# Kernel tuning notes

Measured on AMD Instinct MI355X. Metric: run time of the kernel, lower is better.

## Reference

```python
import math
import jax, jax.numpy as jnp
import numpy as np

B, T, J, EMBED, W = 16, 243, 17, 256, 3  # D = EMBED + 1 = 257, KW = 2*W+1 = 7


def log_map0_spatial(x):
    """Lorentz log map at origin (curvature 1), returning the spatial part.
    x: [..., d+1] points on the hyperboloid. Equals log_map0(x)[..., 1:]."""
    x_t = x[..., :1]
    x_s = x[..., 1:]
    xn = jnp.clip(jnp.linalg.norm(x_s, axis=-1, keepdims=True), 1e-7, None)
    return jnp.arccosh(jnp.maximum(x_t, 1.0 + 1e-7)) / xn * x_s


def exp_map0(v):
    """Lorentz exp map at origin. v: [..., d+1] tangent vector (time comp 0)."""
    v_s = v[..., 1:]
    n = jnp.clip(jnp.linalg.norm(v_s, axis=-1, keepdims=True), 1e-7, None)
    return jnp.concatenate([jnp.cosh(n), jnp.sinh(n) / n * v_s], axis=-1)


def setup_inputs() -> dict:
    key = jax.random.key(0)
    ks = jax.random.split(key, 8)
    # valid hyperboloid points: time = sqrt(1 + ||spatial||^2)
    s = jax.random.normal(ks[0], (B, T, J, EMBED), jnp.float32) * 0.5
    t = jnp.sqrt(1.0 + jnp.sum(s * s, axis=-1, keepdims=True))
    x_seq = jnp.concatenate([t, s], axis=-1)  # [B,T,J,D]
    vel_seq = jax.random.normal(ks[1], (B, T, J, EMBED + 1), jnp.float32) * 0.1
    sc = 1.0 / math.sqrt(EMBED)
    Wq = jax.random.normal(ks[2], (EMBED, EMBED), jnp.float32) * sc
    Wk = jax.random.normal(ks[3], (EMBED, EMBED), jnp.float32) * sc
    Wv = jax.random.normal(ks[4], (EMBED, EMBED), jnp.float32) * sc
    bq = jax.random.normal(ks[5], (EMBED,), jnp.float32) * sc
    bk = jax.random.normal(ks[6], (EMBED,), jnp.float32) * sc
    bv = jax.random.normal(ks[7], (EMBED,), jnp.float32) * sc
    tau = jnp.ones((1,), jnp.float32)
    return {"x_seq": x_seq, "vel_seq": vel_seq, "tau": tau,
            "Wq": Wq, "bq": bq, "Wk": Wk, "bk": bk, "Wv": Wv, "bv": bv}


def reference(x_seq, vel_seq, tau, Wq, bq, Wk, bk, Wv, bv):
    Bb, Tt, Jj, D = x_seq.shape
    d = D - 1
    KW = 2 * W + 1
    # [B,T,J,D] -> [B*J, T, D]
    x_flat = jnp.transpose(x_seq, (0, 2, 1, 3)).reshape(Bb * Jj, Tt, D)
    spatial = log_map0_spatial(x_flat)  # [BJ, T, d]
    q = spatial @ Wq.T + bq
    k = spatial @ Wk.T + bk
    v = spatial @ Wv.T + bv
    # replicate-pad along time, build +/-W windows (fixed small loop over KW=7)
    k_pad = jnp.pad(k, ((0, 0), (W, W), (0, 0)), mode='edge')
    v_pad = jnp.pad(v, ((0, 0), (W, W), (0, 0)), mode='edge')
    k_win = jnp.stack([k_pad[:, i:i + Tt] for i in range(KW)], axis=2)  # [BJ,T,KW,d]
    v_win = jnp.stack([v_pad[:, i:i + Tt] for i in range(KW)], axis=2)
    tau_c = jnp.maximum(tau, 0.001)  # shape [1], broadcasts
    logits = jnp.einsum('btd,btwd->btw', q, k_win) / (math.sqrt(d) * tau_c)
    # mask out-of-range frames at the temporal boundaries
    frame_idx = jnp.arange(Tt)[:, None] + (jnp.arange(KW) - W)[None, :]
    boundary = (frame_idx < 0) | (frame_idx >= Tt)  # [T,KW]
    logits = jnp.where(boundary[None], -jnp.inf, logits)
    attn = jax.nn.softmax(logits, axis=-1)  # [BJ,T,KW]
    agg = jnp.einsum('btw,btwd->btd', attn, v_win)  # [BJ,T,d]
    agg_full = jnp.pad(agg, ((0, 0), (0, 0), (1, 0)))  # prepend zero time comp
    z = exp_map0(agg_full)  # [BJ,T,D]
    return jnp.transpose(z.reshape(Bb, Jj, Tt, D), (0, 2, 1, 3))
```

## Files before the change

### kernel.cpp

```cpp
#include <hip/hip_runtime.h>
#include <hip/hip_bf16.h>

#define B_   16
#define T_   243
#define J_   17
#define E_   256
#define D_   257
#define BJ_  (B_ * J_)
#define M_   (BJ_ * T_)

typedef __bf16 bf16x8 __attribute__((ext_vector_type(8)));
typedef float  f32x4  __attribute__((ext_vector_type(4)));

static __device__ __forceinline__ float bf2f(unsigned short u) {
  unsigned int v = ((unsigned int)u) << 16;
  return __builtin_bit_cast(float, v);
}
static __device__ __forceinline__ unsigned short f2bf(float f) {
  __hip_bfloat16 h = __float2bfloat16(f);
  return __builtin_bit_cast(unsigned short, h);
}
static __device__ __forceinline__ float wave_sum(float v) {
  v += __shfl_xor(v, 1);
  v += __shfl_xor(v, 2);
  v += __shfl_xor(v, 4);
  v += __shfl_xor(v, 8);
  v += __shfl_xor(v, 16);
  v += __shfl_xor(v, 32);
  return v;
}
static __device__ __forceinline__ void gload_lds16(const void* g, void* l) {
  __builtin_amdgcn_global_load_lds(
      (const __attribute__((address_space(1))) void*)g,
      (__attribute__((address_space(3))) void*)l, 16, 0, 0);
}

__global__ void fuse_w_kernel(const float* __restrict__ Wq,
                              const float* __restrict__ Wk,
                              const float* __restrict__ Wv,
                              __hip_bfloat16* __restrict__ wf) {
  int idx = blockIdx.x * 256 + threadIdx.x;
  float v = (idx < 65536) ? Wq[idx]
          : (idx < 131072) ? Wk[idx - 65536]
                           : Wv[idx - 131072];
  ((unsigned short*)wf)[idx] = f2bf(v);
}

__global__ __launch_bounds__(512) void qkv_fused_kernel(
    const float* __restrict__ x, const unsigned short* __restrict__ Wf,
    const float* __restrict__ bq, const float* __restrict__ bk,
    const float* __restrict__ bv, unsigned short* __restrict__ C) {
  __shared__ __align__(16) unsigned short lA[128 * 256];
  __shared__ __align__(16) unsigned short lW[2][128 * 64];

  int tid  = threadIdx.x;
  int w    = tid >> 6;
  int lane = tid & 63;
  int wr   = w >> 2;
  int wcn  = w & 3;
  int m0   = blockIdx.x * 128;

  {
    char* bA = (char*)lA;
    for (int rr = 0; rr < 16; ++rr) {
      int lr = w * 16 + rr;
      int m  = m0 + lr; if (m > M_ - 1) m = M_ - 1;
      int bj = m / T_;  int t = m - bj * T_;
      int b  = bj / J_; int j = bj - b * J_;
      const float* row = x + (size_t)((b * T_ + t) * J_ + j) * D_;
      float xs[4], ss = 0.f;
#pragma unroll
      for (int i = 0; i < 4; ++i) {
        xs[i] = row[1 + lane * 4 + i];
        ss += xs[i] * xs[i];
      }
      ss = wave_sum(ss);
      float xn = fmaxf(sqrtf(ss), 1e-7f);
      float alpha = acoshf(fmaxf(row[0], 1.f + 1e-7f)) / xn;
      ushort4 o;
      o.x = f2bf(xs[0] * alpha); o.y = f2bf(xs[1] * alpha);
      o.z = f2bf(xs[2] * alpha); o.w = f2bf(xs[3] * alpha);
      int byte = lr * 512 + ((lane * 8) ^ ((lr & 7) << 4));
      *(ushort4*)(bA + byte) = o;
    }
  }
  __syncthreads();

  int rowInWave = lane >> 3;
  int srcSlot   = (lane & 7) ^ rowInWave;

  const char* bA = (const char*)lA;

  for (int nt = 0; nt < 6; ++nt) {
    int n0 = nt * 128;

    float bias[2];
#pragma unroll
    for (int ni = 0; ni < 2; ++ni) {
      int colg = n0 + wcn * 32 + ni * 16 + (lane & 15);
      bias[ni] = (colg < 256) ? bq[colg]
               : (colg < 512) ? bk[colg - 256] : bv[colg - 512];
    }

    f32x4 acc[4][2] = {};

#pragma unroll
    for (int i = 0; i < 2; ++i) {
      int rbase = (w * 2 + i) * 8;
      gload_lds16(Wf + (size_t)(n0 + rbase + rowInWave) * 256 + srcSlot * 8,
                  lW[0] + rbase * 64);
    }
    __syncthreads();

    for (int kk = 0; kk < 4; ++kk) {
      if (kk < 3) {
#pragma unroll
        for (int i = 0; i < 2; ++i) {
          int rbase = (w * 2 + i) * 8;
          gload_lds16(Wf + (size_t)(n0 + rbase + rowInWave) * 256 +
                          (kk + 1) * 64 + srcSlot * 8,
                      lW[(kk + 1) & 1] + rbase * 64);
        }
      }
      const char* bW = (const char*)lW[kk & 1];
#pragma unroll
      for (int ki = 0; ki < 2; ++ki) {
        bf16x8 a[4], bfr[2];
        int cbA = kk * 128 + ki * 64 + (lane >> 4) * 16;
#pragma unroll
        for (int mi = 0; mi < 4; ++mi) {
          int r = wr * 64 + mi * 16 + (lane & 15);
          a[mi] = *(const bf16x8*)(bA + r * 512 + (cbA ^ ((r & 7) << 4)));
        }
        int cbB = ki * 64 + (lane >> 4) * 16;
#pragma unroll
        for (int ni = 0; ni < 2; ++ni) {
          int r = wcn * 32 + ni * 16 + (lane & 15);
          bfr[ni] = *(const bf16x8*)(bW + r * 128 + (cbB ^ ((r & 7) << 4)));
        }
#pragma unroll
        for (int mi = 0; mi < 4; ++mi)
#pragma unroll
          for (int ni = 0; ni < 2; ++ni)
            acc[mi][ni] = __builtin_amdgcn_mfma_f32_16x16x32_bf16(
                a[mi], bfr[ni], acc[mi][ni], 0, 0, 0);
      }
      __syncthreads();
    }

    char* bC = (char*)lW[0];
#pragma unroll
    for (int mi = 0; mi < 4; ++mi)
#pragma unroll
      for (int ni = 0; ni < 2; ++ni) {
        int col = wcn * 32 + ni * 16 + (lane & 15);
#pragma unroll
        for (int r = 0; r < 4; ++r) {
          int row  = wr * 64 + mi * 16 + (lane >> 4) * 4 + r;
          int byte = row * 256 + ((col * 2) ^ ((row & 7) << 4));
          *(unsigned short*)(bC + byte) = f2bf(acc[mi][ni][r] + bias[ni]);
        }
      }
    __syncthreads();
#pragma unroll
    for (int p = 0; p < 4; ++p) {
      int row  = p * 32 + (tid >> 4);
      int seg  = tid & 15;
      int byte = row * 256 + ((seg * 16) ^ ((row & 7) << 4));
      uint4 val = *(const uint4*)(bC + byte);
      int gm = m0 + row;
      if (gm < M_)
        *(uint4*)(C + (size_t)gm * 768 + n0 + seg * 8) = val;
    }
    __syncthreads();
  }
}

__global__ __launch_bounds__(256) void attn_kernel(
    const unsigned short* __restrict__ qkv, const float* __restrict__ tau,
    float* __restrict__ out) {
  int wid  = threadIdx.x >> 6;
  int lane = threadIdx.x & 63;
  int t = blockIdx.x * 4 + wid;
  if (t >= T_) return;
  int bj = blockIdx.y;
  int b = bj / J_, j = bj % J_;
  size_t mrow = (size_t)bj * T_ + t;

  float tauc = fmaxf(tau[0], 1e-3f);
  float sc = 1.f / (16.f * tauc);

  float q[4];
  {
    ushort4 qa = *(const ushort4*)(qkv + mrow * 768 + lane * 4);
    q[0] = bf2f(qa.x); q[1] = bf2f(qa.y); q[2] = bf2f(qa.z); q[3] = bf2f(qa.w);
  }

  float logit[7];
#pragma unroll
  for (int ww = 0; ww < 7; ++ww) {
    int t2 = t + ww - 3;
    float d = -INFINITY;
    if (t2 >= 0 && t2 < T_) {
      size_t m2 = (size_t)bj * T_ + t2;
      ushort4 ka = *(const ushort4*)(qkv + m2 * 768 + 256 + lane * 4);
      float p = q[0] * bf2f(ka.x) + q[1] * bf2f(ka.y) +
                q[2] * bf2f(ka.z) + q[3] * bf2f(ka.w);
      d = wave_sum(p) * sc;
    }
    logit[ww] = d;
  }

  float mx = logit[0];
#pragma unroll
  for (int ww = 1; ww < 7; ++ww) mx = fmaxf(mx, logit[ww]);
  float e[7], s = 0.f;
#pragma unroll
  for (int ww = 0; ww < 7; ++ww) {
    e[ww] = expf(logit[ww] - mx);
    s += e[ww];
  }
  float inv = 1.f / s;

  float agg[4] = {0.f, 0.f, 0.f, 0.f};
#pragma unroll
  for (int ww = 0; ww < 7; ++ww) {
    int t2 = t + ww - 3;
    if (t2 >= 0 && t2 < T_) {
      size_t m2 = (size_t)bj * T_ + t2;
      ushort4 va = *(const ushort4*)(qkv + m2 * 768 + 512 + lane * 4);
      agg[0] += e[ww] * bf2f(va.x);
      agg[1] += e[ww] * bf2f(va.y);
      agg[2] += e[ww] * bf2f(va.z);
      agg[3] += e[ww] * bf2f(va.w);
    }
  }
#pragma unroll
  for (int i = 0; i < 4; ++i) agg[i] *= inv;

  float nn = agg[0]*agg[0] + agg[1]*agg[1] + agg[2]*agg[2] + agg[3]*agg[3];
  nn = wave_sum(nn);
  float n = fmaxf(sqrtf(nn), 1e-7f);
  float scale = sinhf(n) / n;

  float* orow = out + ((size_t)(b * T_ + t) * J_ + j) * D_;
  if (lane == 0) orow[0] = coshf(n);
#pragma unroll
  for (int i = 0; i < 4; ++i) orow[1 + lane * 4 + i] = agg[i] * scale;
}

extern "C" void kernel_launch(void* const* d_in, const int* in_sizes, int n_in,
                              void* d_out, int out_size, void* d_ws, size_t ws_size,
                              hipStream_t stream) {
  const float* x   = (const float*)d_in[0];
  const float* tau = (const float*)d_in[2];
  const float* Wq  = (const float*)d_in[3];
  const float* bq  = (const float*)d_in[4];
  const float* Wk  = (const float*)d_in[5];
  const float* bk  = (const float*)d_in[6];
  const float* Wv  = (const float*)d_in[7];
  const float* bv  = (const float*)d_in[8];
  float* out = (float*)d_out;

  char* ws = (char*)d_ws;
  __hip_bfloat16* wf  = (__hip_bfloat16*)(ws);
  unsigned short* qkv = (unsigned short*)(ws + 393216);

  fuse_w_kernel<<<dim3(768), dim3(256), 0, stream>>>(Wq, Wk, Wv, wf);
  qkv_fused_kernel<<<dim3(517), dim3(512), 0, stream>>>(
      x, (const unsigned short*)wf, bq, bk, bv, qkv);
  attn_kernel<<<dim3(61, BJ_), dim3(256), 0, stream>>>(qkv, tau, out);
}
```

Baseline: 343.3 us.

## Halve GEMM row tile and loop attention waves over 16 timesteps

The QKV GEMM now uses 64-row tiles with 256 threads, doubling the grid so more CUs get work and each block needs less LDS. The attention kernel gives each wave a run of 16 consecutive timesteps, clamps window indices so it can load all K and V rows without branches, and writes the output as float4. Reloading overlapping window rows within one wave is meant to hit cache and cut launch overhead, but the attention grid shrinks to 4x272 blocks with a serial loop, which may underfill the GPU.

```diff
diff --git a/kernel.cpp b/kernel.cpp
--- a/kernel.cpp
+++ b/kernel.cpp
@@ -46,19 +46,19 @@
   ((unsigned short*)wf)[idx] = f2bf(v);
 }
 
-__global__ __launch_bounds__(512) void qkv_fused_kernel(
+__global__ __launch_bounds__(256) void qkv_gemm_kernel(
     const float* __restrict__ x, const unsigned short* __restrict__ Wf,
     const float* __restrict__ bq, const float* __restrict__ bk,
     const float* __restrict__ bv, unsigned short* __restrict__ C) {
-  __shared__ __align__(16) unsigned short lA[128 * 256];
+  __shared__ __align__(16) unsigned short lA[64 * 256];
   __shared__ __align__(16) unsigned short lW[2][128 * 64];
 
   int tid  = threadIdx.x;
   int w    = tid >> 6;
   int lane = tid & 63;
-  int wr   = w >> 2;
-  int wcn  = w & 3;
-  int m0   = blockIdx.x * 128;
+  int wr   = w >> 1;
+  int wcn  = w & 1;
+  int m0   = blockIdx.x * 64;
 
   {
     char* bA = (char*)lA;
@@ -94,19 +94,19 @@
   for (int nt = 0; nt < 6; ++nt) {
     int n0 = nt * 128;
 
-    float bias[2];
-#pragma unroll
-    for (int ni = 0; ni < 2; ++ni) {
-      int colg = n0 + wcn * 32 + ni * 16 + (lane & 15);
+    float bias[4];
+#pragma unroll
+    for (int ni = 0; ni < 4; ++ni) {
+      int colg = n0 + wcn * 64 + ni * 16 + (lane & 15);
       bias[ni] = (colg < 256) ? bq[colg]
                : (colg < 512) ? bk[colg - 256] : bv[colg - 512];
     }
 
-    f32x4 acc[4][2] = {};
-
-#pragma unroll
-    for (int i = 0; i < 2; ++i) {
-      int rbase = (w * 2 + i) * 8;
+    f32x4 acc[2][4] = {};
+
+#pragma unroll
+    for (int i = 0; i < 4; ++i) {
+      int rbase = (w * 4 + i) * 8;
       gload_lds16(Wf + (size_t)(n0 + rbase + rowInWave) * 256 + srcSlot * 8,
                   lW[0] + rbase * 64);
     }
@@ -115,8 +115,8 @@
     for (int kk = 0; kk < 4; ++kk) {
       if (kk < 3) {
 #pragma unroll
-        for (int i = 0; i < 2; ++i) {
-          int rbase = (w * 2 + i) * 8;
+        for (int i = 0; i < 4; ++i) {
+          int rbase = (w * 4 + i) * 8;
           gload_lds16(Wf + (size_t)(n0 + rbase + rowInWave) * 256 +
                           (kk + 1) * 64 + srcSlot * 8,
                       lW[(kk + 1) & 1] + rbase * 64);
@@ -125,23 +125,23 @@
       const char* bW = (const char*)lW[kk & 1];
 #pragma unroll
       for (int ki = 0; ki < 2; ++ki) {
-        bf16x8 a[4], bfr[2];
+        bf16x8 a[2], bfr[4];
         int cbA = kk * 128 + ki * 64 + (lane >> 4) * 16;
 #pragma unroll
-        for (int mi = 0; mi < 4; ++mi) {
-          int r = wr * 64 + mi * 16 + (lane & 15);
+        for (int mi = 0; mi < 2; ++mi) {
+          int r = wr * 32 + mi * 16 + (lane & 15);
           a[mi] = *(const bf16x8*)(bA + r * 512 + (cbA ^ ((r & 7) << 4)));
         }
         int cbB = ki * 64 + (lane >> 4) * 16;
 #pragma unroll
-        for (int ni = 0; ni < 2; ++ni) {
-          int r = wcn * 32 + ni * 16 + (lane & 15);
+        for (int ni = 0; ni < 4; ++ni) {
+          int r = wcn * 64 + ni * 16 + (lane & 15);
           bfr[ni] = *(const bf16x8*)(bW + r * 128 + (cbB ^ ((r & 7) << 4)));
         }
 #pragma unroll
-        for (int mi = 0; mi < 4; ++mi)
-#pragma unroll
-          for (int ni = 0; ni < 2; ++ni)
+        for (int mi = 0; mi < 2; ++mi)
+#pragma unroll
+          for (int ni = 0; ni < 4; ++ni)
             acc[mi][ni] = __builtin_amdgcn_mfma_f32_16x16x32_bf16(
                 a[mi], bfr[ni], acc[mi][ni], 0, 0, 0);
       }
@@ -150,13 +150,13 @@
 
     char* bC = (char*)lW[0];
 #pragma unroll
-    for (int mi = 0; mi < 4; ++mi)
-#pragma unroll
-      for (int ni = 0; ni < 2; ++ni) {
-        int col = wcn * 32 + ni * 16 + (lane & 15);
+    for (int mi = 0; mi < 2; ++mi)
+#pragma unroll
+      for (int ni = 0; ni < 4; ++ni) {
+        int col = wcn * 64 + ni * 16 + (lane & 15);
 #pragma unroll
         for (int r = 0; r < 4; ++r) {
-          int row  = wr * 64 + mi * 16 + (lane >> 4) * 4 + r;
+          int row  = wr * 32 + mi * 16 + (lane >> 4) * 4 + r;
           int byte = row * 256 + ((col * 2) ^ ((row & 7) << 4));
           *(unsigned short*)(bC + byte) = f2bf(acc[mi][ni][r] + bias[ni]);
         }
@@ -164,7 +164,7 @@
     __syncthreads();
 #pragma unroll
     for (int p = 0; p < 4; ++p) {
-      int row  = p * 32 + (tid >> 4);
+      int row  = p * 16 + (tid >> 4);
       int seg  = tid & 15;
       int byte = row * 256 + ((seg * 16) ^ ((row & 7) << 4));
       uint4 val = *(const uint4*)(bC + byte);
@@ -181,72 +181,70 @@
     float* __restrict__ out) {
   int wid  = threadIdx.x >> 6;
   int lane = threadIdx.x & 63;
-  int t = blockIdx.x * 4 + wid;
-  if (t >= T_) return;
+  int c  = blockIdx.x * 4 + wid;
+  int t0 = c * 16;
+  int t1 = min(T_, t0 + 16);
   int bj = blockIdx.y;
   int b = bj / J_, j = bj % J_;
-  size_t mrow = (size_t)bj * T_ + t;
+  const unsigned short* base = qkv + (size_t)bj * T_ * 768;
 
   float tauc = fmaxf(tau[0], 1e-3f);
   float sc = 1.f / (16.f * tauc);
 
-  float q[4];
-  {
-    ushort4 qa = *(const ushort4*)(qkv + mrow * 768 + lane * 4);
-    q[0] = bf2f(qa.x); q[1] = bf2f(qa.y); q[2] = bf2f(qa.z); q[3] = bf2f(qa.w);
+  for (int t = t0; t < t1; ++t) {
+    ushort4 qa = *(const ushort4*)(base + (size_t)t * 768 + lane * 4);
+    ushort4 ka[7], va[7];
+#pragma unroll
+    for (int ww = 0; ww < 7; ++ww) {
+      int t2 = t + ww - 3;
+      int tc = min(max(t2, 0), T_ - 1);
+      const unsigned short* rowp = base + (size_t)tc * 768;
+      ka[ww] = *(const ushort4*)(rowp + 256 + lane * 4);
+      va[ww] = *(const ushort4*)(rowp + 512 + lane * 4);
+    }
+    float q0 = bf2f(qa.x), q1 = bf2f(qa.y), q2 = bf2f(qa.z), q3 = bf2f(qa.w);
+
+    float logit[7];
+#pragma unroll
+    for (int ww = 0; ww < 7; ++ww) {
+      float p = q0 * bf2f(ka[ww].x) + q1 * bf2f(ka[ww].y) +
+                q2 * bf2f(ka[ww].z) + q3 * bf2f(ka[ww].w);
+      p = wave_sum(p) * sc;
+      int t2 = t + ww - 3;
+      logit[ww] = (t2 < 0 || t2 >= T_) ? -INFINITY : p;
+    }
+
+    float mx = logit[0];
+#pragma unroll
+    for (int ww = 1; ww < 7; ++ww) mx = fmaxf(mx, logit[ww]);
+    float e[7], s = 0.f;
+#pragma unroll
+    for (int ww = 0; ww < 7; ++ww) {
+      e[ww] = expf(logit[ww] - mx);
+      s += e[ww];
+    }
+    float inv = 1.f / s;
+
+    float ag0 = 0.f, ag1 = 0.f, ag2 = 0.f, ag3 = 0.f;
+#pragma unroll
+    for (int ww = 0; ww < 7; ++ww) {
+      ag0 += e[ww] * bf2f(va[ww].x);
+      ag1 += e[ww] * bf2f(va[ww].y);
+      ag2 += e[ww] * bf2f(va[ww].z);
+      ag3 += e[ww] * bf2f(va[ww].w);
+    }
+    ag0 *= inv; ag1 *= inv; ag2 *= inv; ag3 *= inv;
+
+    float nn = wave_sum(ag0*ag0 + ag1*ag1 + ag2*ag2 + ag3*ag3);
+    float n = fmaxf(sqrtf(nn), 1e-7f);
+    float scale = sinhf(n) / n;
+
+    float* orow = out + ((size_t)(b * T_ + t) * J_ + j) * D_;
+    if (lane == 0) orow[0] = coshf(n);
+    float4 o; o.x = ag0 * scale; o.y = ag1 * scale;
+    o.z = ag2 * scale; o.w = ag3 * scale;
+    *(float4*)(orow + 1 + lane * 4) = o;
   }
-
-  float logit[7];
-#pragma unroll
-  for (int ww = 0; ww < 7; ++ww) {
-    int t2 = t + ww - 3;
-    float d = -INFINITY;
-    if (t2 >= 0 && t2 < T_) {
-      size_t m2 = (size_t)bj * T_ + t2;
-      ushort4 ka = *(const ushort4*)(qkv + m2 * 768 + 256 + lane * 4);
-      float p = q[0] * bf2f(ka.x) + q[1] * bf2f(ka.y) +
-                q[2] * bf2f(ka.z) + q[3] * bf2f(ka.w);
-      d = wave_sum(p) * sc;
-    }
-    logit[ww] = d;
-  }
-
-  float mx = logit[0];
-#pragma unroll
-  for (int ww = 1; ww < 7; ++ww) mx = fmaxf(mx, logit[ww]);
-  float e[7], s = 0.f;
-#pragma unroll
-  for (int ww = 0; ww < 7; ++ww) {
-    e[ww] = expf(logit[ww] - mx);
-    s += e[ww];
-  }
-  float inv = 1.f / s;
-
-  float agg[4] = {0.f, 0.f, 0.f, 0.f};
-#pragma unroll
-  for (int ww = 0; ww < 7; ++ww) {
-    int t2 = t + ww - 3;
-    if (t2 >= 0 && t2 < T_) {
-      size_t m2 = (size_t)bj * T_ + t2;
-      ushort4 va = *(const ushort4*)(qkv + m2 * 768 + 512 + lane * 4);
-      agg[0] += e[ww] * bf2f(va.x);
-      agg[1] += e[ww] * bf2f(va.y);
-      agg[2] += e[ww] * bf2f(va.z);
-      agg[3] += e[ww] * bf2f(va.w);
-    }
-  }
-#pragma unroll
-  for (int i = 0; i < 4; ++i) agg[i] *= inv;
-
-  float nn = agg[0]*agg[0] + agg[1]*agg[1] + agg[2]*agg[2] + agg[3]*agg[3];
-  nn = wave_sum(nn);
-  float n = fmaxf(sqrtf(nn), 1e-7f);
-  float scale = sinhf(n) / n;
-
-  float* orow = out + ((size_t)(b * T_ + t) * J_ + j) * D_;
-  if (lane == 0) orow[0] = coshf(n);
-#pragma unroll
-  for (int i = 0; i < 4; ++i) orow[1 + lane * 4 + i] = agg[i] * scale;
 }
 
 extern "C" void kernel_launch(void* const* d_in, const int* in_sizes, int n_in,
@@ -267,7 +265,7 @@
   unsigned short* qkv = (unsigned short*)(ws + 393216);
 
   fuse_w_kernel<<<dim3(768), dim3(256), 0, stream>>>(Wq, Wk, Wv, wf);
-  qkv_fused_kernel<<<dim3(517), dim3(512), 0, stream>>>(
+  qkv_gemm_kernel<<<dim3(1034), dim3(256), 0, stream>>>(
       x, (const unsigned short*)wf, bq, bk, bv, qkv);
-  attn_kernel<<<dim3(61, BJ_), dim3(256), 0, stream>>>(qkv, tau, out);
-}
+  attn_kernel<<<dim3(4, BJ_), dim3(256), 0, stream>>>(qkv, tau, out);
+}
```

New measurement: 321.6 us. 1.07x faster.
